# Optimization experiments

Hardware: AMD Instinct MI355X
Metric: run time of the kernel (lower is better)

## Reference

```python
import jax, jax.numpy as jnp
import numpy as np

EPS = 1e-6

def layernorm(x, gamma, beta):
    mu = jnp.mean(x, axis=-1, keepdims=True)
    var = jnp.mean((x - mu) ** 2, axis=-1, keepdims=True)
    return (x - mu) * jax.lax.rsqrt(var + EPS) * gamma + beta

def setup_inputs() -> dict:
    key = jax.random.key(0)
    ks = jax.random.split(key, 9)
    B, S, D, F = 8, 4096, 768, 3072
    inputs = jax.random.normal(ks[0], (B, S, D), dtype=jnp.float32)
    W1 = jax.random.normal(ks[1], (D, F), dtype=jnp.float32) * (1.0 / np.sqrt(D))
    b1 = jnp.zeros((F,), dtype=jnp.float32)
    W2 = jax.random.normal(ks[2], (F, D), dtype=jnp.float32) * (1.0 / np.sqrt(F))
    b2 = jnp.zeros((D,), dtype=jnp.float32)
    gamma1 = jnp.ones((D,), dtype=jnp.float32)
    beta1 = jnp.zeros((D,), dtype=jnp.float32)
    gamma2 = jnp.ones((D,), dtype=jnp.float32)
    beta2 = jnp.zeros((D,), dtype=jnp.float32)
    return {"inputs": inputs, "W1": W1, "b1": b1, "W2": W2, "b2": b2,
            "gamma1": gamma1, "beta1": beta1, "gamma2": gamma2, "beta2": beta2}

def reference(inputs, W1, b1, W2, b2, gamma1, beta1, gamma2, beta2):
    # Fourier token mixing: complex 2D FFT over (seq, embed), keep real part
    attn = jnp.real(jnp.fft.fft2(inputs.astype(jnp.complex64), axes=(-2, -1))).astype(jnp.float32)
    out1 = layernorm(inputs + attn, gamma1, beta1)
    # FFN: Dense(gelu) -> Dense
    h = jax.nn.gelu(out1 @ W1 + b1, approximate=False)
    ffn = h @ W2 + b2
    return layernorm(out1 + ffn, gamma2, beta2)
```

## Files before the change

### kernel.cpp

```cpp
#include <hip/hip_runtime.h>
#include <cstdint>


typedef __attribute__((ext_vector_type(8))) short short8;
typedef __attribute__((ext_vector_type(4))) float f32x4;

__device__ __forceinline__ unsigned short f2b(float f) {
  union { float f; uint32_t u; } c; c.f = f;
  uint32_t u = c.u;
  u += 0x7FFFu + ((u >> 16) & 1u);
  return (unsigned short)(u >> 16);
}
__device__ __forceinline__ float b2f(unsigned short h) {
  union { uint32_t u; float f; } c; c.u = ((uint32_t)h) << 16;
  return c.f;
}

__device__ __forceinline__ float gelu_fast(float x) {
  float x2 = x * x;
  float inner = x * fmaf(x2, 0.0356774081f, 0.7978845608f);
  float zz = fminf(inner * 2.885390082f, 80.0f);
  float E, r;
  asm("v_exp_f32 %0, %1" : "=v"(E) : "v"(zz));
  float den = E + 1.0f;
  asm("v_rcp_f32 %0, %1" : "=v"(r) : "v"(den));
  return x * E * r;
}


__global__ __launch_bounds__(256) void f32_to_bf16_vec(
    const float* __restrict__ in, unsigned short* __restrict__ out) {
  long i = (long)blockIdx.x * 256 + threadIdx.x;
  float4 v = reinterpret_cast<const float4*>(in)[i];
  ushort4 o;
  o.x = f2b(v.x); o.y = f2b(v.y); o.z = f2b(v.z); o.w = f2b(v.w);
  reinterpret_cast<ushort4*>(out)[i] = o;
}

__global__ __launch_bounds__(256) void fill_bt1(unsigned short* __restrict__ Bt1) {
  int i = blockIdx.x * 256 + threadIdx.x;
  int j = i / 768;
  int n = i - j * 768;
  int jj = j & 511;
  int m = (jj * n) % 768;
  float ang = (float)m * (6.283185307179586f / 768.0f);
  Bt1[i] = f2b((j < 512) ? cosf(ang) : sinf(ang));
}

__global__ __launch_bounds__(256) void fill_auv(
    unsigned short* __restrict__ Au, unsigned short* __restrict__ Av) {
  long i = (long)blockIdx.x * 256 + threadIdx.x;
  int k = (int)(i >> 12);
  int s = (int)(i & 4095);
  int mm = (k * s) & 4095;
  float ang = (float)mm * (6.283185307179586f / 4096.0f);
  Au[i] = f2b(cosf(ang));
  Av[i] = f2b(sinf(ang));
}

__global__ __launch_bounds__(256) void transpose_f32_to_bf16(
    const float* __restrict__ in, unsigned short* __restrict__ out, int R, int C) {
  __shared__ float tile[32][33];
  const int c0 = blockIdx.x * 32;
  const int r0 = blockIdx.y * 32;
  const int tx = threadIdx.x & 31;
  const int ty = threadIdx.x >> 5;
#pragma unroll
  for (int i = ty; i < 32; i += 8)
    tile[i][tx] = in[(long)(r0 + i) * C + c0 + tx];
  __syncthreads();
#pragma unroll
  for (int i = ty; i < 32; i += 8)
    out[(long)(c0 + i) * R + r0 + tx] = f2b(tile[tx][i]);
}


template <int EPI>
__global__ __launch_bounds__(256, 3) void gemm128(
    const unsigned short* __restrict__ A, const unsigned short* __restrict__ Bt,
    const unsigned short* __restrict__ A2p, const unsigned short* __restrict__ Bt2p,
    int K, int lda, int ldb, long bBatch, long oBatch, int zSplit,
    int NX, int NY,
    float* __restrict__ outF,
    unsigned short* __restrict__ outB, unsigned short* __restrict__ outB2,
    const float* __restrict__ bias, const unsigned short* __restrict__ residB,
    int ldOut) {
  __shared__ __align__(16) unsigned short As[128 * 64];
  __shared__ __align__(16) unsigned short Bs[128 * 64];

  const int tid = threadIdx.x;
  const int lane = tid & 63;
  const int wave = tid >> 6;
  const int wr = wave >> 1;
  const int wc = wave & 1;

  const int p = (int)blockIdx.x;
  const int l = (p & 7) * ((int)gridDim.x >> 3) + (p >> 3);
  const int by = l % NY;
  const int lx = l / NY;
  const int bx = lx % NX;
  int zz = lx / NX;

  const unsigned short* Ax = A;
  const unsigned short* Bx = Bt;
  unsigned short* oB = outB;
  if (EPI == 1 && zz >= zSplit) { Ax = A2p; Bx = Bt2p; oB = outB2; zz -= zSplit; }

  const unsigned short* Ab = Ax + (long)bx * 128 * lda;
  const unsigned short* Bb = Bx + (long)zz * bBatch + (long)by * 128 * ldb;

  const int NT = K >> 6;

  const int srow = lane >> 3;
  const int scolE = ((lane & 7) ^ srow) << 3;

  const int fr = lane & 15;
  const int fkB = (lane >> 4) << 4;
  const int fxor = (lane & 7) << 4;

  f32x4 acc[4][4] = {};

  for (int t = 0; t < NT; ++t) {
#pragma unroll
    for (int i_ = 0; i_ < 4; ++i_) {
      const int chunk = i_ * 4 + wave;
      const int row = chunk * 8 + srow;
      __builtin_amdgcn_global_load_lds(
          (const __attribute__((address_space(1))) void*)(Ab + (long)row * lda + (long)t * 64 + scolE),
          (__attribute__((address_space(3))) void*)(As + chunk * 512), 16, 0, 0);
      __builtin_amdgcn_global_load_lds(
          (const __attribute__((address_space(1))) void*)(Bb + (long)row * ldb + (long)t * 64 + scolE),
          (__attribute__((address_space(3))) void*)(Bs + chunk * 512), 16, 0, 0);
    }
    __syncthreads();

    const char* Ap = reinterpret_cast<const char*>(As);
    const char* Bp = reinterpret_cast<const char*>(Bs);
#pragma unroll
    for (int ks = 0; ks < 2; ++ks) {
      short8 af[4], bf[4];
#pragma unroll
      for (int mf = 0; mf < 4; ++mf) {
        const int row = wr * 64 + mf * 16 + fr;
        af[mf] = *reinterpret_cast<const short8*>(Ap + ((row * 128 + ks * 64 + fkB) ^ fxor));
      }
#pragma unroll
      for (int nf = 0; nf < 4; ++nf) {
        const int row = wc * 64 + nf * 16 + fr;
        bf[nf] = *reinterpret_cast<const short8*>(Bp + ((row * 128 + ks * 64 + fkB) ^ fxor));
      }
#pragma unroll
      for (int mf = 0; mf < 4; ++mf)
#pragma unroll
        for (int nf = 0; nf < 4; ++nf)
          acc[mf][nf] = __builtin_amdgcn_mfma_f32_16x16x32_bf16(
              af[mf], bf[nf], acc[mf][nf], 0, 0, 0);
    }
    __syncthreads();
  }

  const long rowBase = (long)bx * 128 + wr * 64 + ((lane >> 4) << 2);
  const int colBase = by * 128 + wc * 64 + (lane & 15);
#pragma unroll
  for (int mf = 0; mf < 4; ++mf) {
#pragma unroll
    for (int nf = 0; nf < 4; ++nf) {
      const int col = colBase + nf * 16;
#pragma unroll
      for (int i = 0; i < 4; ++i) {
        const long r = rowBase + mf * 16 + i;
        float vv = acc[mf][nf][i];
        if constexpr (EPI == 0) {
          const long dst = (long)(col >> 9) * 16777216L +
                           ((((long)(r >> 12) << 9) + (col & 511)) << 12) + (r & 4095);
          outB[dst] = f2b(vv);
        } else if constexpr (EPI == 1) {
          oB[(long)zz * oBatch + r * (long)ldOut + col] = f2b(vv);
        } else if constexpr (EPI == 2) {
          outB[r * (long)ldOut + col] = f2b(gelu_fast(vv + bias[col]));
        } else {
          const long idx = r * (long)ldOut + col;
          outF[idx] = vv + bias[col] + b2f(residB[idx]);
        }
      }
    }
  }
}

__global__ __launch_bounds__(256) void combine_ln(
    const unsigned short* __restrict__ u, const unsigned short* __restrict__ v,
    const unsigned short* __restrict__ xb, const float* __restrict__ gamma,
    const float* __restrict__ beta, unsigned short* __restrict__ o1b) {
  const int k = blockIdx.x;
  const int z = blockIdx.y;
  const long ub = ((long)z * 2304 + k) * 512;
  const long base = (long)z * 4096L * 768;
  const long rowA = base + (long)k * 768;
  const long rowB = base + (long)(4096 - k) * 768;
  const bool doRowB = (k != 0) && (k != 2048);
  const int t = threadIdx.x;

  float vA0[2], vA1[2], vB0[2], vB1[2];
  float sA = 0.f, qA = 0.f, sB = 0.f, qB = 0.f;
#pragma unroll
  for (int it = 0; it < 2; ++it) {
    const int d = t + it * 256;
    if (d <= 384) {
      const float uu = b2f(u[ub + d]);
      const float vv = b2f(v[ub + d]);
      const float a1 = uu - vv;
      const float a2 = uu + vv;
      const int dd = 768 - d;
      const bool colB = (d != 0) && (d != 384);
      float va = a1 + b2f(xb[rowA + d]);
      vA0[it] = va; sA += va; qA += va * va;
      if (colB) { float w = a2 + b2f(xb[rowA + dd]); vA1[it] = w; sA += w; qA += w * w; }
      if (doRowB) {
        float wb = a2 + b2f(xb[rowB + d]);
        vB0[it] = wb; sB += wb; qB += wb * wb;
        if (colB) { float w2 = a1 + b2f(xb[rowB + dd]); vB1[it] = w2; sB += w2; qB += w2 * w2; }
      }
    }
  }
#pragma unroll
  for (int off = 32; off > 0; off >>= 1) {
    sA += __shfl_down(sA, off, 64); qA += __shfl_down(qA, off, 64);
    sB += __shfl_down(sB, off, 64); qB += __shfl_down(qB, off, 64);
  }
  __shared__ float red[4][4];
  if ((t & 63) == 0) {
    red[t >> 6][0] = sA; red[t >> 6][1] = qA;
    red[t >> 6][2] = sB; red[t >> 6][3] = qB;
  }
  __syncthreads();
  const float SA = red[0][0] + red[1][0] + red[2][0] + red[3][0];
  const float QA = red[0][1] + red[1][1] + red[2][1] + red[3][1];
  const float SB = red[0][2] + red[1][2] + red[2][2] + red[3][2];
  const float QB = red[0][3] + red[1][3] + red[2][3] + red[3][3];
  const float muA = SA * (1.0f / 768.0f);
  const float rsA = rsqrtf(QA * (1.0f / 768.0f) - muA * muA + 1e-6f);
  const float muB = SB * (1.0f / 768.0f);
  const float rsB = rsqrtf(QB * (1.0f / 768.0f) - muB * muB + 1e-6f);

#pragma unroll
  for (int it = 0; it < 2; ++it) {
    const int d = t + it * 256;
    if (d <= 384) {
      const int dd = 768 - d;
      const bool colB = (d != 0) && (d != 384);
      const float g0 = gamma[d], b0 = beta[d];
      o1b[rowA + d] = f2b((vA0[it] - muA) * rsA * g0 + b0);
      if (colB) o1b[rowA + dd] = f2b((vA1[it] - muA) * rsA * gamma[dd] + beta[dd]);
      if (doRowB) {
        o1b[rowB + d] = f2b((vB0[it] - muB) * rsB * g0 + b0);
        if (colB) o1b[rowB + dd] = f2b((vB1[it] - muB) * rsB * gamma[dd] + beta[dd]);
      }
    }
  }
}

__global__ __launch_bounds__(256) void ln_row_f32(
    const float* __restrict__ in, const float* __restrict__ gamma,
    const float* __restrict__ beta, float* __restrict__ outF) {
  const long row = blockIdx.x;
  const float* p = in + row * 768;
  const int t = threadIdx.x;
  const float v0 = p[t], v1 = p[t + 256], v2 = p[t + 512];
  float s = v0 + v1 + v2;
  float q = v0 * v0 + v1 * v1 + v2 * v2;
#pragma unroll
  for (int off = 32; off > 0; off >>= 1) {
    s += __shfl_down(s, off, 64);
    q += __shfl_down(q, off, 64);
  }
  __shared__ float ss[4], sq[4];
  if ((t & 63) == 0) { ss[t >> 6] = s; sq[t >> 6] = q; }
  __syncthreads();
  const float S = ss[0] + ss[1] + ss[2] + ss[3];
  const float Q = sq[0] + sq[1] + sq[2] + sq[3];
  const float mu = S * (1.0f / 768.0f);
  const float var = Q * (1.0f / 768.0f) - mu * mu;
  const float rs = rsqrtf(var + 1e-6f);
  outF[row * 768 + t]       = (v0 - mu) * rs * gamma[t] + beta[t];
  outF[row * 768 + t + 256] = (v1 - mu) * rs * gamma[t + 256] + beta[t + 256];
  outF[row * 768 + t + 512] = (v2 - mu) * rs * gamma[t + 512] + beta[t + 512];
}


extern "C" void kernel_launch(void* const* d_in, const int* in_sizes, int n_in,
                              void* d_out, int out_size, void* d_ws, size_t ws_size,
                              hipStream_t stream) {
  const float* x   = (const float*)d_in[0];
  const float* W1  = (const float*)d_in[1];
  const float* b1  = (const float*)d_in[2];
  const float* W2  = (const float*)d_in[3];
  const float* b2  = (const float*)d_in[4];
  const float* g1  = (const float*)d_in[5];
  const float* be1 = (const float*)d_in[6];
  const float* g2  = (const float*)d_in[7];
  const float* be2 = (const float*)d_in[8];
  float* out = (float*)d_out;

  char* ws = (char*)d_ws;
  unsigned short* xb   = (unsigned short*)(ws + 0L);
  unsigned short* Bt1  = (unsigned short*)(ws + 50331648L);
  unsigned short* Au   = (unsigned short*)(ws + 51904512L);
  unsigned short* Av   = (unsigned short*)(ws + 70778880L);
  unsigned short* u_b  = (unsigned short*)(ws + 89653248L);
  unsigned short* v_b  = (unsigned short*)(ws + 108527616L);
  unsigned short* BtUV = (unsigned short*)(ws + 156762112L);
  unsigned short* H    = (unsigned short*)(ws + 0L);
  unsigned short* o1b  = (unsigned short*)(ws + 201326592L);
  unsigned short* W1t  = (unsigned short*)(ws + 251658240L);
  unsigned short* W2t  = (unsigned short*)(ws + 256376832L);

  f32_to_bf16_vec<<<24576, 256, 0, stream>>>(x, xb);
  fill_bt1<<<3072, 256, 0, stream>>>(Bt1);
  fill_auv<<<36864, 256, 0, stream>>>(Au, Av);
  transpose_f32_to_bf16<<<dim3(96, 24), 256, 0, stream>>>(W1, W1t, 768, 3072);
  transpose_f32_to_bf16<<<dim3(24, 96), 256, 0, stream>>>(W2, W2t, 3072, 768);

  gemm128<0><<<2048, 256, 0, stream>>>(
      xb, Bt1, nullptr, nullptr, 768, 768, 768, 0L, 0L, 999, 256, 8,
      nullptr, BtUV, nullptr, nullptr, nullptr, 0);

  gemm128<1><<<1152, 256, 0, stream>>>(
      Au, BtUV, Av, BtUV + 16777216L, 4096, 4096, 4096,
      512L * 4096L, 2304L * 512L, 8, 18, 4,
      nullptr, u_b, v_b, nullptr, nullptr, 512);

  combine_ln<<<dim3(2049, 8), 256, 0, stream>>>(u_b, v_b, xb, g1, be1, o1b);

  gemm128<2><<<6144, 256, 0, stream>>>(
      o1b, W1t, nullptr, nullptr, 768, 768, 768, 0L, 0L, 999, 256, 24,
      nullptr, H, nullptr, b1, nullptr, 3072);

  gemm128<3><<<1536, 256, 0, stream>>>(
      H, W2t, nullptr, nullptr, 3072, 3072, 3072, 0L, 0L, 999, 256, 6,
      out, nullptr, nullptr, b2, o1b, 768);

  ln_row_f32<<<32768, 256, 0, stream>>>(out, g2, be2, out);
}
```

Measured before the change: 722.3 us.

## Fold sequence axis by real-input symmetry to halve the DFT GEMM sizes

Adds an xfold kernel that forms s+(4096-s) sums and differences (cos and sin parts) of the input rows, so the sequence-axis DFT uses K=2176 instead of 4096. The first DFT GEMM now splits into separate cosine and sine halves, and the second GEMM shrinks along both K and M. This exploits real-input even/odd symmetry to cut GEMM FLOPs and twiddle-table size roughly in half, at the cost of a new fold pass and zero padding. It also adds grouped column-block scheduling (NG) to the GEMM tile mapping, used as a 2-way grouping for the FFN1 GEMM.

New measurement: 661.0 us. 1.09x faster.

```diff
diff --git a/kernel.cpp b/kernel.cpp
--- a/kernel.cpp
+++ b/kernel.cpp
@@ -27,14 +27,33 @@
   return x * E * r;
 }
 
-
-__global__ __launch_bounds__(256) void f32_to_bf16_vec(
-    const float* __restrict__ in, unsigned short* __restrict__ out) {
-  long i = (long)blockIdx.x * 256 + threadIdx.x;
-  float4 v = reinterpret_cast<const float4*>(in)[i];
-  ushort4 o;
-  o.x = f2b(v.x); o.y = f2b(v.y); o.z = f2b(v.z); o.w = f2b(v.w);
-  reinterpret_cast<ushort4*>(out)[i] = o;
+__global__ __launch_bounds__(256) void xfold(
+    const float* __restrict__ x, unsigned short* __restrict__ xb,
+    unsigned short* __restrict__ xc, unsigned short* __restrict__ xs) {
+  const int k = blockIdx.x;
+  const int b = blockIdx.y;
+  const long xbase = (long)b * 4096 * 768;
+  const long cbase = (long)b * 2176 * 768;
+  const int t = threadIdx.x;
+#pragma unroll
+  for (int it = 0; it < 3; ++it) {
+    const int c = t + it * 256;
+    const float a = x[xbase + (long)k * 768 + c];
+    xb[xbase + (long)k * 768 + c] = f2b(a);
+    if (k == 0 || k == 2048) {
+      xc[cbase + (long)k * 768 + c] = f2b(a);
+      xs[cbase + (long)k * 768 + c] = 0;
+    } else {
+      const float bb = x[xbase + (long)(4096 - k) * 768 + c];
+      xb[xbase + (long)(4096 - k) * 768 + c] = f2b(bb);
+      xc[cbase + (long)k * 768 + c] = f2b(a + bb);
+      xs[cbase + (long)k * 768 + c] = f2b(a - bb);
+    }
+    if (k >= 1 && k <= 127) {
+      xc[cbase + (long)(2048 + k) * 768 + c] = 0;
+      xs[cbase + (long)(2048 + k) * 768 + c] = 0;
+    }
+  }
 }
 
 __global__ __launch_bounds__(256) void fill_bt1(unsigned short* __restrict__ Bt1) {
@@ -50,8 +69,9 @@
 __global__ __launch_bounds__(256) void fill_auv(
     unsigned short* __restrict__ Au, unsigned short* __restrict__ Av) {
   long i = (long)blockIdx.x * 256 + threadIdx.x;
-  int k = (int)(i >> 12);
-  int s = (int)(i & 4095);
+  if (i >= 2176L * 2176L) return;
+  int k = (int)(i / 2176);
+  int s = (int)(i - (long)k * 2176);
   int mm = (k * s) & 4095;
   float ang = (float)mm * (6.283185307179586f / 4096.0f);
   Au[i] = f2b(cosf(ang));
@@ -80,7 +100,7 @@
     const unsigned short* __restrict__ A, const unsigned short* __restrict__ Bt,
     const unsigned short* __restrict__ A2p, const unsigned short* __restrict__ Bt2p,
     int K, int lda, int ldb, long bBatch, long oBatch, int zSplit,
-    int NX, int NY,
+    int NX, int NYG, int NG,
     float* __restrict__ outF,
     unsigned short* __restrict__ outB, unsigned short* __restrict__ outB2,
     const float* __restrict__ bias, const unsigned short* __restrict__ residB,
@@ -96,15 +116,17 @@
 
   const int p = (int)blockIdx.x;
   const int l = (p & 7) * ((int)gridDim.x >> 3) + (p >> 3);
-  const int by = l % NY;
-  const int lx = l / NY;
-  const int bx = lx % NX;
-  int zz = lx / NX;
+  int rem = l;
+  const int byg = rem % NYG; rem /= NYG;
+  const int bx  = rem % NX;  rem /= NX;
+  const int g   = rem % NG;  rem /= NG;
+  int zz = rem;
+  const int by = g * NYG + byg;
 
   const unsigned short* Ax = A;
   const unsigned short* Bx = Bt;
   unsigned short* oB = outB;
-  if (EPI == 1 && zz >= zSplit) { Ax = A2p; Bx = Bt2p; oB = outB2; zz -= zSplit; }
+  if ((EPI == 0 || EPI == 1) && zz >= zSplit) { Ax = A2p; Bx = Bt2p; oB = outB2; zz -= zSplit; }
 
   const unsigned short* Ab = Ax + (long)bx * 128 * lda;
   const unsigned short* Bb = Bx + (long)zz * bBatch + (long)by * 128 * ldb;
@@ -171,9 +193,10 @@
         const long r = rowBase + mf * 16 + i;
         float vv = acc[mf][nf][i];
         if constexpr (EPI == 0) {
-          const long dst = (long)(col >> 9) * 16777216L +
-                           ((((long)(r >> 12) << 9) + (col & 511)) << 12) + (r & 4095);
-          outB[dst] = f2b(vv);
+          const int rr = (int)r;
+          const int bz = rr / 2176;
+          const int sp = rr - bz * 2176;
+          oB[((long)(bz * 512 + col)) * 2176 + sp] = f2b(vv);
         } else if constexpr (EPI == 1) {
           oB[(long)zz * oBatch + r * (long)ldOut + col] = f2b(vv);
         } else if constexpr (EPI == 2) {
@@ -193,7 +216,7 @@
     const float* __restrict__ beta, unsigned short* __restrict__ o1b) {
   const int k = blockIdx.x;
   const int z = blockIdx.y;
-  const long ub = ((long)z * 2304 + k) * 512;
+  const long ub = ((long)z * 2176 + k) * 512;
   const long base = (long)z * 4096L * 768;
   const long rowA = base + (long)k * 768;
   const long rowB = base + (long)(4096 - k) * 768;
@@ -305,38 +328,41 @@
   unsigned short* xb   = (unsigned short*)(ws + 0L);
   unsigned short* Bt1  = (unsigned short*)(ws + 50331648L);
   unsigned short* Au   = (unsigned short*)(ws + 51904512L);
-  unsigned short* Av   = (unsigned short*)(ws + 70778880L);
-  unsigned short* u_b  = (unsigned short*)(ws + 89653248L);
-  unsigned short* v_b  = (unsigned short*)(ws + 108527616L);
-  unsigned short* BtUV = (unsigned short*)(ws + 156762112L);
+  unsigned short* Av   = (unsigned short*)(ws + 61374464L);
+  unsigned short* xc   = (unsigned short*)(ws + 70844416L);
+  unsigned short* xs   = (unsigned short*)(ws + 97583104L);
+  unsigned short* BtU  = (unsigned short*)(ws + 124321792L);
+  unsigned short* BtV  = (unsigned short*)(ws + 142147584L);
+  unsigned short* u_b  = (unsigned short*)(ws + 159973376L);
+  unsigned short* v_b  = (unsigned short*)(ws + 177799168L);
   unsigned short* H    = (unsigned short*)(ws + 0L);
   unsigned short* o1b  = (unsigned short*)(ws + 201326592L);
   unsigned short* W1t  = (unsigned short*)(ws + 251658240L);
   unsigned short* W2t  = (unsigned short*)(ws + 256376832L);
 
-  f32_to_bf16_vec<<<24576, 256, 0, stream>>>(x, xb);
+  xfold<<<dim3(2049, 8), 256, 0, stream>>>(x, xb, xc, xs);
   fill_bt1<<<3072, 256, 0, stream>>>(Bt1);
-  fill_auv<<<36864, 256, 0, stream>>>(Au, Av);
+  fill_auv<<<18496, 256, 0, stream>>>(Au, Av);
   transpose_f32_to_bf16<<<dim3(96, 24), 256, 0, stream>>>(W1, W1t, 768, 3072);
   transpose_f32_to_bf16<<<dim3(24, 96), 256, 0, stream>>>(W2, W2t, 3072, 768);
 
-  gemm128<0><<<2048, 256, 0, stream>>>(
-      xb, Bt1, nullptr, nullptr, 768, 768, 768, 0L, 0L, 999, 256, 8,
-      nullptr, BtUV, nullptr, nullptr, nullptr, 0);
-
-  gemm128<1><<<1152, 256, 0, stream>>>(
-      Au, BtUV, Av, BtUV + 16777216L, 4096, 4096, 4096,
-      512L * 4096L, 2304L * 512L, 8, 18, 4,
+  gemm128<0><<<1088, 256, 0, stream>>>(
+      xc, Bt1, xs, Bt1 + 512 * 768, 768, 768, 768, 0L, 0L, 1, 136, 4, 1,
+      nullptr, BtU, BtV, nullptr, nullptr, 0);
+
+  gemm128<1><<<1088, 256, 0, stream>>>(
+      Au, BtU, Av, BtV, 2176, 2176, 2176,
+      512L * 2176L, 2176L * 512L, 8, 17, 4, 1,
       nullptr, u_b, v_b, nullptr, nullptr, 512);
 
   combine_ln<<<dim3(2049, 8), 256, 0, stream>>>(u_b, v_b, xb, g1, be1, o1b);
 
   gemm128<2><<<6144, 256, 0, stream>>>(
-      o1b, W1t, nullptr, nullptr, 768, 768, 768, 0L, 0L, 999, 256, 24,
+      o1b, W1t, nullptr, nullptr, 768, 768, 768, 0L, 0L, 999, 256, 12, 2,
       nullptr, H, nullptr, b1, nullptr, 3072);
 
   gemm128<3><<<1536, 256, 0, stream>>>(
-      H, W2t, nullptr, nullptr, 3072, 3072, 3072, 0L, 0L, 999, 256, 6,
+      H, W2t, nullptr, nullptr, 3072, 3072, 3072, 0L, 0L, 999, 256, 6, 1,
       out, nullptr, nullptr, b2, o1b, 768);
 
   ln_row_f32<<<32768, 256, 0, stream>>>(out, g2, be2, out);
```
